# Performance work log

Measured on AMD Instinct MI355X. Metric: run time of the kernel, lower is better.

Reference implementation:

```python
import jax, jax.numpy as jnp
import numpy as np

N_NODES = 100000
N_EDGES = 1600000
D_IN = 64
D_HID = 64
D_OUT = 64
TOPK = 32


def _num_params(din, dout):
    return din * dout + dout


def setup_inputs() -> dict:
    key = jax.random.key(0)
    ks = jax.random.split(key, 16)
    x = jax.random.normal(ks[0], (N_NODES, D_IN), dtype=jnp.float32)
    edge_index = jax.random.randint(ks[1], (2, N_EDGES), 0, N_NODES, dtype=jnp.int64)
    # GCN layer params (PyG GCNConv: lin.weight [out,in], bias [out])
    w0 = jax.random.normal(ks[2], (D_HID, D_IN), dtype=jnp.float32) * (1.0 / np.sqrt(D_IN))
    b0 = jnp.zeros((D_HID,), dtype=jnp.float32)
    w1 = jax.random.normal(ks[3], (D_OUT, D_HID), dtype=jnp.float32) * (1.0 / np.sqrt(D_HID))
    b1 = jnp.zeros((D_OUT,), dtype=jnp.float32)
    # summarization vectors p (torch.randn init)
    p0 = jax.random.normal(ks[4], (D_IN,), dtype=jnp.float32)
    p1 = jax.random.normal(ks[5], (D_HID,), dtype=jnp.float32)
    # GRU cells: hidden = num_params, input = topk * feature_dim
    np0 = _num_params(D_IN, D_HID)
    np1 = _num_params(D_HID, D_OUT)
    gi0 = TOPK * D_IN
    gi1 = TOPK * D_HID
    s0 = 1.0 / np.sqrt(np0)
    s1 = 1.0 / np.sqrt(np1)
    wih0 = jax.random.uniform(ks[6], (3 * np0, gi0), jnp.float32, -s0, s0)
    whh0 = jax.random.uniform(ks[7], (3 * np0, np0), jnp.float32, -s0, s0)
    bih0 = jax.random.uniform(ks[8], (3 * np0,), jnp.float32, -s0, s0)
    bhh0 = jax.random.uniform(ks[9], (3 * np0,), jnp.float32, -s0, s0)
    wih1 = jax.random.uniform(ks[10], (3 * np1, gi1), jnp.float32, -s1, s1)
    whh1 = jax.random.uniform(ks[11], (3 * np1, np1), jnp.float32, -s1, s1)
    bih1 = jax.random.uniform(ks[12], (3 * np1,), jnp.float32, -s1, s1)
    bhh1 = jax.random.uniform(ks[13], (3 * np1,), jnp.float32, -s1, s1)
    return {"x": x, "edge_index": edge_index,
            "p0": p0, "p1": p1,
            "w0": w0, "b0": b0, "w1": w1, "b1": b1,
            "wih0": wih0, "whh0": whh0, "bih0": bih0, "bhh0": bhh0,
            "wih1": wih1, "whh1": whh1, "bih1": bih1, "bhh1": bhh1}


def _summarize(h, p, k):
    # attention summary: top-k nodes by h @ p_norm, weighted by tanh(score)
    p_norm = p / (jnp.linalg.norm(p) + 1e-8)
    y = h @ p_norm                      # [N]
    _, idx = jax.lax.top_k(y, k)        # k <= N here, matches torch.topk branch
    w = jnp.tanh(y)
    return h[idx] * w[idx][:, None]     # [k, feat]


def _gru_cell(xv, hv, wih, whh, bih, bhh):
    gi = xv @ wih.T + bih
    gh = hv @ whh.T + bhh
    ir, iz, inew = jnp.split(gi, 3)
    hr, hz, hnew = jnp.split(gh, 3)
    r = jax.nn.sigmoid(ir + hr)
    z = jax.nn.sigmoid(iz + hz)
    n = jnp.tanh(inew + r * hnew)
    return (1.0 - z) * n + z * hv


def _gcn_conv(h, src, dst, weight, bias, n_nodes):
    # PyG GCNConv: x' = x @ W.T; add self-loops; sym-norm aggregation; + bias
    xw = h @ weight.T
    loop = jnp.arange(n_nodes, dtype=src.dtype)
    s = jnp.concatenate([src, loop])
    d = jnp.concatenate([dst, loop])
    deg = jax.ops.segment_sum(jnp.ones(s.shape[0], dtype=xw.dtype), d,
                              num_segments=n_nodes)
    dinv = jnp.where(deg > 0, jax.lax.rsqrt(jnp.maximum(deg, 1e-12)), 0.0)
    norm = dinv[s] * dinv[d]
    msgs = xw[s] * norm[:, None]
    out = jax.ops.segment_sum(msgs, d, num_segments=n_nodes)
    return out + bias


def reference(x, edge_index, p0, p1, w0, b0, w1, b1,
              wih0, whh0, bih0, bhh0, wih1, whh1, bih1, bhh1):
    src, dst = edge_index[0], edge_index[1]
    n = x.shape[0]
    h = x
    layers = [
        (p0, w0, b0, wih0, whh0, bih0, bhh0, D_IN, D_HID, True),
        (p1, w1, b1, wih1, whh1, bih1, bhh1, D_HID, D_OUT, False),
    ]
    for (p, w, b, wih, whh, bih, bhh, din, dout, relu) in layers:
        # summarize node embeddings -> GRU input (Z_t.T.flatten(): feature-major)
        Z = _summarize(h, p, TOPK)                  # [TOPK, din]
        z_flat = Z.T.reshape(-1)                    # [din*TOPK]
        # initial GRU hidden = flattened current GCN params (weight then bias)
        h0 = jnp.concatenate([w.reshape(-1), b])    # [din*dout + dout]
        new_w = _gru_cell(z_flat, h0, wih, whh, bih, bhh)
        weight = new_w[: din * dout].reshape(dout, din)
        bias = new_w[din * dout:]
        h = _gcn_conv(h, src, dst, weight, bias, n)
        if relu:
            h = jax.nn.relu(h)  # dropout is identity in eval mode
    return h
```

## Files before the change

kernel.cpp:

```cpp
#include <hip/hip_runtime.h>
#include <math.h>

#define N_NODES 100000
#define N_EDGES 1600000
#define D 64
#define NP 4160
#define GI3 12480
#define GIN 2048
#define TOPK 32
#define SCAN_BLKS 98

#define OFF_PN     0u
#define OFF_MISC   64u
#define OFF_IDX    80u
#define OFF_WSEL   112u
#define OFF_ZFLAT  144u
#define OFF_NEWW   2192u
#define OFF_GI     6400u
#define OFF_GH     18880u
#define OFF_HIST   31360u
#define OFF_Y      96896u
#define OFF_DEG    196896u
#define OFF_DINV   296896u
#define OFF_ROWPTR 396896u
#define OFF_CURSOR 496898u
#define OFF_COL    596898u
#define OFF_CAND   2196898u
#define OFF_XW     2396898u
#define OFF_H1     8796898u
#define OFF_BSUM   15196898u
#define WS_FLOATS  15197026u

__device__ __forceinline__ unsigned fkey(float f) {
    unsigned u = __float_as_uint(f);
    return u ^ ((u & 0x80000000u) ? 0xFFFFFFFFu : 0x80000000u);
}

__global__ void k_zero32(unsigned* __restrict__ p, int n) {
    int i = blockIdx.x * blockDim.x + threadIdx.x;
    if (i < n) p[i] = 0u;
}

__global__ void k_count(const int* __restrict__ dst, unsigned* __restrict__ deg, int ne) {
    int i = blockIdx.x * blockDim.x + threadIdx.x;
    if (i < ne) atomicAdd(&deg[dst[i]], 1u);
}

__global__ void k_dinv(const unsigned* __restrict__ deg, float* __restrict__ dinv, int n) {
    int i = blockIdx.x * blockDim.x + threadIdx.x;
    if (i < n) dinv[i] = rsqrtf((float)(deg[i] + 1u));
}

__global__ void k_scanA(const unsigned* __restrict__ deg, unsigned* __restrict__ bsum, int n) {
    __shared__ unsigned s[256];
    int t = threadIdx.x;
    int base = blockIdx.x * 1024 + t * 4;
    unsigned v = 0;
    #pragma unroll
    for (int j = 0; j < 4; ++j) { int i = base + j; if (i < n) v += deg[i]; }
    s[t] = v; __syncthreads();
    for (int off = 128; off; off >>= 1) {
        if (t < off) s[t] += s[t + off];
        __syncthreads();
    }
    if (t == 0) bsum[blockIdx.x] = s[0];
}

__global__ void k_scanB(unsigned* __restrict__ bsum, unsigned* __restrict__ rowptr, int nb, int n) {
    __shared__ unsigned s[128];
    int t = threadIdx.x;
    unsigned v = (t < nb) ? bsum[t] : 0u;
    s[t] = v; __syncthreads();
    for (int off = 1; off < 128; off <<= 1) {
        unsigned a = (t >= off) ? s[t - off] : 0u;
        __syncthreads();
        s[t] += a;
        __syncthreads();
    }
    if (t < nb) bsum[t] = s[t] - v;
    if (t == 127) rowptr[n] = s[127];
}

__global__ void k_scanC(const unsigned* __restrict__ deg, const unsigned* __restrict__ bsum,
                        unsigned* __restrict__ rowptr, unsigned* __restrict__ cursor, int n) {
    __shared__ unsigned s[256];
    int t = threadIdx.x;
    int base = blockIdx.x * 1024 + t * 4;
    unsigned loc[4]; unsigned v = 0;
    #pragma unroll
    for (int j = 0; j < 4; ++j) { int i = base + j; loc[j] = (i < n) ? deg[i] : 0u; v += loc[j]; }
    s[t] = v; __syncthreads();
    for (int off = 1; off < 256; off <<= 1) {
        unsigned a = (t >= off) ? s[t - off] : 0u;
        __syncthreads();
        s[t] += a;
        __syncthreads();
    }
    unsigned run = bsum[blockIdx.x] + s[t] - v;
    #pragma unroll
    for (int j = 0; j < 4; ++j) {
        int i = base + j;
        if (i < n) { rowptr[i] = run; cursor[i] = run; run += loc[j]; }
    }
}

__global__ void k_fill(const int* __restrict__ src, const int* __restrict__ dst,
                       unsigned* __restrict__ cursor, int* __restrict__ col, int ne) {
    int i = blockIdx.x * blockDim.x + threadIdx.x;
    if (i < ne) {
        unsigned pos = atomicAdd(&cursor[dst[i]], 1u);
        col[pos] = src[i];
    }
}

__global__ void k_pnorm(const float* __restrict__ p, float* __restrict__ pn,
                        unsigned* __restrict__ misc) {
    int t = threadIdx.x;
    float v = p[t];
    float s = v * v;
    for (int o = 32; o; o >>= 1) s += __shfl_down(s, o, 64);
    s = __shfl(s, 0, 64);
    pn[t] = v / (sqrtf(s) + 1e-8f);
    if (t < 16) misc[t] = 0u;
}

__global__ void k_y_hist(const float* __restrict__ h, const float* __restrict__ pn,
                         float* __restrict__ y, unsigned* __restrict__ hist, int n) {
    int wave = (blockIdx.x * blockDim.x + threadIdx.x) >> 6;
    int lane = threadIdx.x & 63;
    int nw = (gridDim.x * blockDim.x) >> 6;
    float p = pn[lane];
    for (int i = wave; i < n; i += nw) {
        float v = h[(size_t)i * D + lane] * p;
        for (int o = 32; o; o >>= 1) v += __shfl_down(v, o, 64);
        if (lane == 0) {
            y[i] = v;
            atomicAdd(&hist[fkey(v) >> 16], 1u);
        }
    }
}

__global__ void k_thresh(const unsigned* __restrict__ hist, unsigned* __restrict__ misc) {
    __shared__ unsigned cs[256];
    __shared__ unsigned s2[256];
    __shared__ int tstar;
    int t = threadIdx.x;
    unsigned sum = 0;
    for (int j = 0; j < 256; ++j) sum += hist[t * 256 + j];
    cs[t] = sum; __syncthreads();
    for (int off = 1; off < 256; off <<= 1) {
        unsigned add = (t + off < 256) ? cs[t + off] : 0u;
        __syncthreads();
        cs[t] += add;
        __syncthreads();
    }
    if (cs[t] >= TOPK && (t == 255 || cs[t + 1] < TOPK)) tstar = t;
    __syncthreads();
    int ts = tstar;
    unsigned above = (ts == 255) ? 0u : cs[ts + 1];
    s2[t] = hist[ts * 256 + t]; __syncthreads();
    for (int off = 1; off < 256; off <<= 1) {
        unsigned add = (t + off < 256) ? s2[t + off] : 0u;
        __syncthreads();
        s2[t] += add;
        __syncthreads();
    }
    if (above + s2[t] >= TOPK && (t == 255 || above + s2[t + 1] < TOPK))
        misc[1] = (unsigned)(ts * 256 + t);
}

__global__ void k_compact(const float* __restrict__ y, unsigned* __restrict__ misc,
                          unsigned long long* __restrict__ cand, int n) {
    int i = blockIdx.x * blockDim.x + threadIdx.x;
    if (i >= n) return;
    unsigned thr = misc[1];
    unsigned k = fkey(y[i]);
    if ((k >> 16) >= thr) {
        unsigned pos = atomicAdd(&misc[0], 1u);
        cand[pos] = ((unsigned long long)k << 32) | (unsigned)(0xFFFFFFFFu - (unsigned)i);
    }
}

__global__ void k_select(const float* __restrict__ y, const unsigned* __restrict__ misc,
                         unsigned long long* __restrict__ cand,
                         int* __restrict__ idxb, float* __restrict__ wsel) {
    int t = threadIdx.x;
    int C = (int)misc[0];
    for (int k = 0; k < TOPK; ++k) {
        unsigned long long m = 0ull;
        for (int j = t; j < C; j += 64) { unsigned long long c = cand[j]; if (c > m) m = c; }
        for (int o = 32; o; o >>= 1) {
            unsigned long long other = __shfl_down(m, o, 64);
            if (other > m) m = other;
        }
        unsigned long long best = __shfl(m, 0, 64);
        for (int j = t; j < C; j += 64) if (cand[j] == best) cand[j] = 0ull;
        if (t == 0) {
            int idx = (int)(0xFFFFFFFFu - (unsigned)(best & 0xFFFFFFFFull));
            idxb[k] = idx;
            wsel[k] = tanhf(y[idx]);
        }
    }
}

__global__ void k_zflat(const float* __restrict__ h, const int* __restrict__ idxb,
                        const float* __restrict__ wsel, float* __restrict__ z) {
    int t = blockIdx.x * blockDim.x + threadIdx.x;
    if (t < GIN) {
        int k = t & 31, d = t >> 5;
        z[t] = h[(size_t)idxb[k] * D + d] * wsel[k];
    }
}

__global__ void k_mv(const float* __restrict__ W, const float* __restrict__ bias,
                     const float* __restrict__ vecA, int lenA, const float* __restrict__ vecB,
                     float* __restrict__ out, int rows, int cols) {
    extern __shared__ float v[];
    for (int j = threadIdx.x; j < cols; j += blockDim.x)
        v[j] = (j < lenA) ? vecA[j] : vecB[j - lenA];
    __syncthreads();
    int wave = (blockIdx.x * blockDim.x + threadIdx.x) >> 6;
    int lane = threadIdx.x & 63;
    if (wave >= rows) return;
    const float4* Wr = (const float4*)(W + (size_t)wave * cols);
    int n4 = cols >> 2;
    float acc = 0.f;
    for (int j = lane; j < n4; j += 64) {
        float4 w4 = Wr[j];
        acc += w4.x * v[4 * j] + w4.y * v[4 * j + 1] + w4.z * v[4 * j + 2] + w4.w * v[4 * j + 3];
    }
    for (int o = 32; o; o >>= 1) acc += __shfl_down(acc, o, 64);
    if (lane == 0) out[wave] = acc + bias[wave];
}

__global__ void k_gru(const float* __restrict__ gi, const float* __restrict__ gh,
                      const float* __restrict__ w, const float* __restrict__ b,
                      float* __restrict__ neww) {
    int j = blockIdx.x * blockDim.x + threadIdx.x;
    if (j >= NP) return;
    float r = 1.f / (1.f + expf(-(gi[j] + gh[j])));
    float z = 1.f / (1.f + expf(-(gi[NP + j] + gh[NP + j])));
    float n = tanhf(gi[2 * NP + j] + r * gh[2 * NP + j]);
    float h0 = (j < 4096) ? w[j] : b[j - 4096];
    neww[j] = (1.f - z) * n + z * h0;
}

__global__ void k_xw(const float* __restrict__ h, const float* __restrict__ neww,
                     float* __restrict__ xw, int n) {
    __shared__ float WT[64 * 64];
    for (int t = threadIdx.x; t < 4096; t += blockDim.x) {
        int o = t >> 6, d = t & 63;
        WT[d * 64 + o] = neww[t];
    }
    __syncthreads();
    int wave = (blockIdx.x * blockDim.x + threadIdx.x) >> 6;
    int lane = threadIdx.x & 63;
    int nw = (gridDim.x * blockDim.x) >> 6;
    for (int i = wave; i < n; i += nw) {
        float hv = h[(size_t)i * D + lane];
        float acc = 0.f;
        #pragma unroll 16
        for (int d = 0; d < 64; ++d) {
            float hd = __shfl(hv, d, 64);
            acc += hd * WT[d * 64 + lane];
        }
        xw[(size_t)i * D + lane] = acc;
    }
}

__global__ void k_agg(const float* __restrict__ xw, const float* __restrict__ dinv,
                      const unsigned* __restrict__ rowptr, const int* __restrict__ col,
                      const float* __restrict__ neww, float* __restrict__ out,
                      int n, int relu) {
    int wave = (blockIdx.x * blockDim.x + threadIdx.x) >> 6;
    int lane = threadIdx.x & 63;
    int nw = (gridDim.x * blockDim.x) >> 6;
    float bias = neww[4096 + lane];
    for (int v = wave; v < n; v += nw) {
        unsigned p0 = rowptr[v], p1 = rowptr[v + 1];
        float dv = dinv[v];
        float acc = dv * xw[(size_t)v * D + lane];
        for (unsigned base = p0; base < p1; base += 64) {
            int cnt = (int)min(64u, p1 - base);
            int s = 0; float ds = 0.f;
            if (lane < cnt) { s = col[base + lane]; ds = dinv[s]; }
            for (int j = 0; j < cnt; ++j) {
                int sj = __shfl(s, j, 64);
                float dsj = __shfl(ds, j, 64);
                acc += dsj * xw[(size_t)sj * D + lane];
            }
        }
        float r = bias + dv * acc;
        if (relu) r = fmaxf(r, 0.f);
        out[(size_t)v * D + lane] = r;
    }
}

extern "C" void kernel_launch(void* const* d_in, const int* in_sizes, int n_in,
                              void* d_out, int out_size, void* d_ws, size_t ws_size,
                              hipStream_t stream) {
    if (ws_size < (size_t)WS_FLOATS * 4) return;

    const float* x = (const float*)d_in[0];
    const int* src = (const int*)d_in[1];
    const int* dst = src + N_EDGES;
    const float* P[2]   = {(const float*)d_in[2],  (const float*)d_in[3]};
    const float* W[2]   = {(const float*)d_in[4],  (const float*)d_in[6]};
    const float* B[2]   = {(const float*)d_in[5],  (const float*)d_in[7]};
    const float* WIH[2] = {(const float*)d_in[8],  (const float*)d_in[12]};
    const float* WHH[2] = {(const float*)d_in[9],  (const float*)d_in[13]};
    const float* BIH[2] = {(const float*)d_in[10], (const float*)d_in[14]};
    const float* BHH[2] = {(const float*)d_in[11], (const float*)d_in[15]};

    float* ws = (float*)d_ws;
    float* pn = ws + OFF_PN;
    unsigned* misc = (unsigned*)(ws + OFF_MISC);
    int* idxb = (int*)(ws + OFF_IDX);
    float* wsel = ws + OFF_WSEL;
    float* zflat = ws + OFF_ZFLAT;
    float* neww = ws + OFF_NEWW;
    float* gi = ws + OFF_GI;
    float* gh = ws + OFF_GH;
    unsigned* hist = (unsigned*)(ws + OFF_HIST);
    float* y = ws + OFF_Y;
    unsigned* deg = (unsigned*)(ws + OFF_DEG);
    float* dinv = ws + OFF_DINV;
    unsigned* rowptr = (unsigned*)(ws + OFF_ROWPTR);
    unsigned* cursor = (unsigned*)(ws + OFF_CURSOR);
    int* col = (int*)(ws + OFF_COL);
    unsigned long long* cand = (unsigned long long*)(ws + OFF_CAND);
    float* xw = ws + OFF_XW;
    float* h1 = ws + OFF_H1;
    unsigned* bsum = (unsigned*)(ws + OFF_BSUM);
    float* out = (float*)d_out;

    hipLaunchKernelGGL(k_zero32, dim3((N_NODES + 255) / 256), dim3(256), 0, stream, deg, N_NODES);
    hipLaunchKernelGGL(k_count, dim3((N_EDGES + 255) / 256), dim3(256), 0, stream, dst, deg, N_EDGES);
    hipLaunchKernelGGL(k_dinv, dim3((N_NODES + 255) / 256), dim3(256), 0, stream, deg, dinv, N_NODES);
    hipLaunchKernelGGL(k_scanA, dim3(SCAN_BLKS), dim3(256), 0, stream, deg, bsum, N_NODES);
    hipLaunchKernelGGL(k_scanB, dim3(1), dim3(128), 0, stream, bsum, rowptr, SCAN_BLKS, N_NODES);
    hipLaunchKernelGGL(k_scanC, dim3(SCAN_BLKS), dim3(256), 0, stream, deg, bsum, rowptr, cursor, N_NODES);
    hipLaunchKernelGGL(k_fill, dim3((N_EDGES + 255) / 256), dim3(256), 0, stream, src, dst, cursor, col, N_EDGES);

    for (int l = 0; l < 2; ++l) {
        const float* h = (l == 0) ? x : h1;
        float* ho = (l == 0) ? h1 : out;
        hipLaunchKernelGGL(k_zero32, dim3(256), dim3(256), 0, stream, hist, 65536);
        hipLaunchKernelGGL(k_pnorm, dim3(1), dim3(64), 0, stream, P[l], pn, misc);
        hipLaunchKernelGGL(k_y_hist, dim3(1024), dim3(256), 0, stream, h, pn, y, hist, N_NODES);
        hipLaunchKernelGGL(k_thresh, dim3(1), dim3(256), 0, stream, hist, misc);
        hipLaunchKernelGGL(k_compact, dim3((N_NODES + 255) / 256), dim3(256), 0, stream, y, misc, cand, N_NODES);
        hipLaunchKernelGGL(k_select, dim3(1), dim3(64), 0, stream, y, misc, cand, idxb, wsel);
        hipLaunchKernelGGL(k_zflat, dim3(8), dim3(256), 0, stream, h, idxb, wsel, zflat);
        hipLaunchKernelGGL(k_mv, dim3(GI3 / 4), dim3(256), GIN * 4, stream,
                           WIH[l], BIH[l], zflat, GIN, zflat, gi, GI3, GIN);
        hipLaunchKernelGGL(k_mv, dim3(GI3 / 4), dim3(256), NP * 4, stream,
                           WHH[l], BHH[l], W[l], 4096, B[l], gh, GI3, NP);
        hipLaunchKernelGGL(k_gru, dim3((NP + 255) / 256), dim3(256), 0, stream, gi, gh, W[l], B[l], neww);
        hipLaunchKernelGGL(k_xw, dim3(2048), dim3(256), 0, stream, h, neww, xw, N_NODES);
        hipLaunchKernelGGL(k_agg, dim3(4096), dim3(256), 0, stream, xw, dinv, rowptr, col, neww, ho,
                           N_NODES, (l == 0) ? 1 : 0);
    }
}
```

Measured before the change: 1.534 ms.

## Build CSR via two-level bucketed scatter instead of global atomics

```diff
diff --git a/kernel.cpp b/kernel.cpp
--- a/kernel.cpp
+++ b/kernel.cpp
@@ -8,7 +8,11 @@
 #define GI3 12480
 #define GIN 2048
 #define TOPK 32
-#define SCAN_BLKS 98
+
+#define NB 391
+#define SCAT_ITEMS 4096
+#define SCAT_BLKS 391
+#define COLCAP 6144
 
 #define OFF_PN     0u
 #define OFF_MISC   64u
@@ -41,76 +45,130 @@
     if (i < n) p[i] = 0u;
 }
 
-__global__ void k_count(const int* __restrict__ dst, unsigned* __restrict__ deg, int ne) {
-    int i = blockIdx.x * blockDim.x + threadIdx.x;
-    if (i < ne) atomicAdd(&deg[dst[i]], 1u);
-}
-
-__global__ void k_dinv(const unsigned* __restrict__ deg, float* __restrict__ dinv, int n) {
-    int i = blockIdx.x * blockDim.x + threadIdx.x;
-    if (i < n) dinv[i] = rsqrtf((float)(deg[i] + 1u));
-}
-
-__global__ void k_scanA(const unsigned* __restrict__ deg, unsigned* __restrict__ bsum, int n) {
-    __shared__ unsigned s[256];
-    int t = threadIdx.x;
-    int base = blockIdx.x * 1024 + t * 4;
-    unsigned v = 0;
+__global__ void k_bcount(const int* __restrict__ dst, unsigned* __restrict__ bcnt, int ne) {
+    __shared__ unsigned h[NB];
+    int t = threadIdx.x;
+    for (int i = t; i < NB; i += 256) h[i] = 0u;
+    __syncthreads();
+    int base0 = blockIdx.x * SCAT_ITEMS;
     #pragma unroll
-    for (int j = 0; j < 4; ++j) { int i = base + j; if (i < n) v += deg[i]; }
-    s[t] = v; __syncthreads();
-    for (int off = 128; off; off >>= 1) {
-        if (t < off) s[t] += s[t + off];
-        __syncthreads();
-    }
-    if (t == 0) bsum[blockIdx.x] = s[0];
-}
-
-__global__ void k_scanB(unsigned* __restrict__ bsum, unsigned* __restrict__ rowptr, int nb, int n) {
-    __shared__ unsigned s[128];
-    int t = threadIdx.x;
-    unsigned v = (t < nb) ? bsum[t] : 0u;
-    s[t] = v; __syncthreads();
-    for (int off = 1; off < 128; off <<= 1) {
-        unsigned a = (t >= off) ? s[t - off] : 0u;
-        __syncthreads();
-        s[t] += a;
-        __syncthreads();
-    }
-    if (t < nb) bsum[t] = s[t] - v;
-    if (t == 127) rowptr[n] = s[127];
-}
-
-__global__ void k_scanC(const unsigned* __restrict__ deg, const unsigned* __restrict__ bsum,
-                        unsigned* __restrict__ rowptr, unsigned* __restrict__ cursor, int n) {
-    __shared__ unsigned s[256];
-    int t = threadIdx.x;
-    int base = blockIdx.x * 1024 + t * 4;
-    unsigned loc[4]; unsigned v = 0;
+    for (int k = 0; k < 16; ++k) {
+        int i = base0 + k * 256 + t;
+        if (i < ne) atomicAdd(&h[dst[i] >> 8], 1u);
+    }
+    __syncthreads();
+    for (int i = t; i < NB; i += 256) if (h[i]) atomicAdd(&bcnt[i], h[i]);
+}
+
+__global__ void k_bscan(const unsigned* __restrict__ bcnt, unsigned* __restrict__ bbase,
+                        unsigned* __restrict__ bcur, unsigned* __restrict__ rowptr) {
+    __shared__ unsigned sc[512];
+    int t = threadIdx.x;
+    unsigned v = (t < NB) ? bcnt[t] : 0u;
+    sc[t] = v; __syncthreads();
+    for (int off = 1; off < 512; off <<= 1) {
+        unsigned a = (t >= off) ? sc[t - off] : 0u;
+        __syncthreads();
+        sc[t] += a;
+        __syncthreads();
+    }
+    unsigned ex = sc[t] - v;
+    if (t <= NB) bbase[t] = ex;
+    if (t < NB) bcur[t] = ex;
+    if (t == 511) rowptr[N_NODES] = sc[511];
+}
+
+__global__ void k_bscatter(const int* __restrict__ src, const int* __restrict__ dst,
+                           unsigned* __restrict__ bcur, unsigned* __restrict__ ebuf, int ne) {
+    __shared__ unsigned hist[NB];
+    __shared__ unsigned sc[512];
+    __shared__ unsigned basel[NB];
+    __shared__ unsigned lcur[NB];
+    __shared__ unsigned gdst[NB];
+    __shared__ unsigned sbuf[SCAT_ITEMS];
+    __shared__ unsigned short sb[SCAT_ITEMS];
+    int t = threadIdx.x;
+    for (int i = t; i < NB; i += 256) hist[i] = 0u;
+    __syncthreads();
+    int base0 = blockIdx.x * SCAT_ITEMS;
+    unsigned key[16]; int bk[16];
     #pragma unroll
-    for (int j = 0; j < 4; ++j) { int i = base + j; loc[j] = (i < n) ? deg[i] : 0u; v += loc[j]; }
-    s[t] = v; __syncthreads();
+    for (int k = 0; k < 16; ++k) {
+        int i = base0 + k * 256 + t;
+        if (i < ne) {
+            int d = dst[i];
+            bk[k] = d >> 8;
+            key[k] = ((unsigned)(d & 255) << 24) | (unsigned)src[i];
+            atomicAdd(&hist[bk[k]], 1u);
+        } else bk[k] = -1;
+    }
+    __syncthreads();
+    {
+        unsigned v0 = hist[t];
+        unsigned v1 = (t + 256 < NB) ? hist[t + 256] : 0u;
+        sc[t] = v0; sc[t + 256] = v1; __syncthreads();
+        for (int off = 1; off < 512; off <<= 1) {
+            unsigned a0 = (t >= off) ? sc[t - off] : 0u;
+            unsigned a1 = (t + 256 >= off) ? sc[t + 256 - off] : 0u;
+            __syncthreads();
+            sc[t] += a0; sc[t + 256] += a1;
+            __syncthreads();
+        }
+    }
+    for (int i = t; i < NB; i += 256) {
+        unsigned b0 = sc[i] - hist[i];
+        basel[i] = b0; lcur[i] = b0;
+    }
+    __syncthreads();
+    for (int i = t; i < NB; i += 256) if (hist[i]) gdst[i] = atomicAdd(&bcur[i], hist[i]);
+    #pragma unroll
+    for (int k = 0; k < 16; ++k) if (bk[k] >= 0) {
+        unsigned p = atomicAdd(&lcur[bk[k]], 1u);
+        sbuf[p] = key[k]; sb[p] = (unsigned short)bk[k];
+    }
+    __syncthreads();
+    int cnt = min(SCAT_ITEMS, ne - base0);
+    for (int j = t; j < cnt; j += 256) {
+        unsigned b = sb[j];
+        ebuf[gdst[b] + ((unsigned)j - basel[b])] = sbuf[j];
+    }
+}
+
+__global__ void k_bcsr(const unsigned* __restrict__ ebuf, const unsigned* __restrict__ bbase,
+                       unsigned* __restrict__ rowptr, float* __restrict__ dinv,
+                       int* __restrict__ col, int n) {
+    __shared__ unsigned deg[256];
+    __shared__ unsigned sc[256];
+    __shared__ unsigned lcur[256];
+    __shared__ int colbuf[COLCAP];
+    int b = blockIdx.x, t = threadIdx.x;
+    int lo = b << 8;
+    unsigned e0 = bbase[b], e1 = bbase[b + 1];
+    deg[t] = 0u; __syncthreads();
+    for (unsigned j = e0 + t; j < e1; j += 256) atomicAdd(&deg[ebuf[j] >> 24], 1u);
+    __syncthreads();
+    sc[t] = deg[t]; __syncthreads();
     for (int off = 1; off < 256; off <<= 1) {
-        unsigned a = (t >= off) ? s[t - off] : 0u;
-        __syncthreads();
-        s[t] += a;
-        __syncthreads();
-    }
-    unsigned run = bsum[blockIdx.x] + s[t] - v;
-    #pragma unroll
-    for (int j = 0; j < 4; ++j) {
-        int i = base + j;
-        if (i < n) { rowptr[i] = run; cursor[i] = run; run += loc[j]; }
-    }
-}
-
-__global__ void k_fill(const int* __restrict__ src, const int* __restrict__ dst,
-                       unsigned* __restrict__ cursor, int* __restrict__ col, int ne) {
-    int i = blockIdx.x * blockDim.x + threadIdx.x;
-    if (i < ne) {
-        unsigned pos = atomicAdd(&cursor[dst[i]], 1u);
-        col[pos] = src[i];
-    }
+        unsigned a = (t >= off) ? sc[t - off] : 0u;
+        __syncthreads();
+        sc[t] += a;
+        __syncthreads();
+    }
+    unsigned lrp = sc[t] - deg[t];
+    if (lo + t < n) {
+        rowptr[lo + t] = e0 + lrp;
+        dinv[lo + t] = rsqrtf((float)(deg[t] + 1u));
+    }
+    lcur[t] = lrp; __syncthreads();
+    for (unsigned j = e0 + t; j < e1; j += 256) {
+        unsigned k = ebuf[j];
+        unsigned p = atomicAdd(&lcur[k >> 24], 1u);
+        if (p < COLCAP) colbuf[p] = (int)(k & 0xFFFFFFu);
+        else col[e0 + p] = (int)(k & 0xFFFFFFu);
+    }
+    __syncthreads();
+    unsigned cnt = e1 - e0;
+    for (unsigned j = t; j < cnt && j < COLCAP; j += 256) col[e0 + j] = colbuf[j];
 }
 
 __global__ void k_pnorm(const float* __restrict__ p, float* __restrict__ pn,
@@ -323,24 +381,23 @@
     float* gh = ws + OFF_GH;
     unsigned* hist = (unsigned*)(ws + OFF_HIST);
     float* y = ws + OFF_Y;
-    unsigned* deg = (unsigned*)(ws + OFF_DEG);
+    unsigned* bcnt  = (unsigned*)(ws + OFF_DEG);
+    unsigned* bbase = (unsigned*)(ws + OFF_DEG) + 512;
+    unsigned* bcur  = (unsigned*)(ws + OFF_DEG) + 1024;
     float* dinv = ws + OFF_DINV;
     unsigned* rowptr = (unsigned*)(ws + OFF_ROWPTR);
-    unsigned* cursor = (unsigned*)(ws + OFF_CURSOR);
     int* col = (int*)(ws + OFF_COL);
     unsigned long long* cand = (unsigned long long*)(ws + OFF_CAND);
     float* xw = ws + OFF_XW;
+    unsigned* ebuf = (unsigned*)(ws + OFF_XW);
     float* h1 = ws + OFF_H1;
-    unsigned* bsum = (unsigned*)(ws + OFF_BSUM);
     float* out = (float*)d_out;
 
-    hipLaunchKernelGGL(k_zero32, dim3((N_NODES + 255) / 256), dim3(256), 0, stream, deg, N_NODES);
-    hipLaunchKernelGGL(k_count, dim3((N_EDGES + 255) / 256), dim3(256), 0, stream, dst, deg, N_EDGES);
-    hipLaunchKernelGGL(k_dinv, dim3((N_NODES + 255) / 256), dim3(256), 0, stream, deg, dinv, N_NODES);
-    hipLaunchKernelGGL(k_scanA, dim3(SCAN_BLKS), dim3(256), 0, stream, deg, bsum, N_NODES);
-    hipLaunchKernelGGL(k_scanB, dim3(1), dim3(128), 0, stream, bsum, rowptr, SCAN_BLKS, N_NODES);
-    hipLaunchKernelGGL(k_scanC, dim3(SCAN_BLKS), dim3(256), 0, stream, deg, bsum, rowptr, cursor, N_NODES);
-    hipLaunchKernelGGL(k_fill, dim3((N_EDGES + 255) / 256), dim3(256), 0, stream, src, dst, cursor, col, N_EDGES);
+    hipLaunchKernelGGL(k_zero32, dim3((NB + 255) / 256), dim3(256), 0, stream, bcnt, NB);
+    hipLaunchKernelGGL(k_bcount, dim3(SCAT_BLKS), dim3(256), 0, stream, dst, bcnt, N_EDGES);
+    hipLaunchKernelGGL(k_bscan, dim3(1), dim3(512), 0, stream, bcnt, bbase, bcur, rowptr);
+    hipLaunchKernelGGL(k_bscatter, dim3(SCAT_BLKS), dim3(256), 0, stream, src, dst, bcur, ebuf, N_EDGES);
+    hipLaunchKernelGGL(k_bcsr, dim3(NB), dim3(256), 0, stream, ebuf, bbase, rowptr, dinv, col, N_NODES);
 
     for (int l = 0; l < 2; ++l) {
         const float* h = (l == 0) ? x : h1;
```

Result: faster. 1.378 ms (-10.1%).
